# Kernel tuning notes

Hardware: AMD Instinct MI355X
Metric: run time of the kernel (lower is better)

## Reference

```python
import jax, jax.numpy as jnp
import numpy as np

J_NUM = 24
# SMPL kinematic tree: parents[i] < i for all i >= 1 (root has parent -1)
PARENTS = np.array([-1, 0, 0, 0, 1, 2, 3, 4, 5, 6, 7, 8, 9, 9, 9, 12, 13, 14,
                    16, 17, 18, 19, 20, 21], dtype=np.int32)
BATCH = 131072


def setup_inputs() -> dict:
    key = jax.random.key(0)
    k1, k2, k3 = jax.random.split(key, 3)
    pose = jax.random.normal(k1, (BATCH, J_NUM, 3), dtype=jnp.float32) * 0.3
    trans = jax.random.normal(k2, (BATCH, 3), dtype=jnp.float32)
    # Rest-pose joint transforms: identity rotation + random local offset (learned buffer)
    offs = jax.random.normal(k3, (J_NUM, 3), dtype=jnp.float32) * 0.1
    J = jnp.tile(jnp.eye(4, dtype=jnp.float32)[None], (J_NUM, 1, 1))
    J = J.at[:, :3, 3].set(offs)
    parents = jnp.asarray(PARENTS, dtype=jnp.int32)
    return {"pose": pose, "trans": trans, "J": J, "parents": parents}


def rodrigues(r):
    """Axis-angle [..., 3] -> rotation matrices [..., 3, 3] (batched Rodrigues)."""
    theta = jnp.sqrt(jnp.sum(r * r, axis=-1, keepdims=True) + 1e-16)  # [...,1]
    rh = r / theta
    x, y, z = rh[..., 0], rh[..., 1], rh[..., 2]
    zero = jnp.zeros_like(x)
    K = jnp.stack([zero, -z, y, z, zero, -x, -y, x, zero], axis=-1)
    K = K.reshape(r.shape[:-1] + (3, 3))
    c = jnp.cos(theta)[..., None]
    s = jnp.sin(theta)[..., None]
    outer = rh[..., :, None] * rh[..., None, :]
    I3 = jnp.eye(3, dtype=r.dtype)
    return c * I3 + (1.0 - c) * outer + s * K


def reference(pose, trans, J, parents):
    par = np.asarray(parents)  # static tree structure
    B, Jn = pose.shape[0], pose.shape[1]
    R = rodrigues(pose)                                   # [B,J,3,3]
    # embed into 4x4 homogeneous transforms
    R4 = jnp.pad(R, ((0, 0), (0, 0), (0, 1), (0, 1)))
    R4 = R4.at[:, :, 3, 3].set(1.0)                       # [B,J,4,4]
    # local transform per joint: J[i] @ localRot[i] (batched once)
    local = jnp.einsum('jab,njbc->njac', J, R4)           # [B,J,4,4]
    # sequential kinematic-tree composition (fixed small unrolled loop)
    results = [local[:, 0]]
    for i in range(1, Jn):
        results.append(jnp.matmul(results[int(par[i])], local[:, i]))
    stacked = jnp.stack(results, axis=1)                  # [B,J,4,4]
    J_posed = stacked[:, :, :3, 3] + trans[:, None, :]    # [B,J,3]
    return J_posed
```

## Files before the change

kernel.cpp:

```cpp
#include <hip/hip_runtime.h>

#define J_NUM 24
#define ELEMS 64
#define NTHREADS (ELEMS * 3)
#define STRIDE 73

__global__ __launch_bounds__(NTHREADS)
void fk_kernel(const float* __restrict__ pose, const float* __restrict__ trans,
               const float* __restrict__ Jm, float* __restrict__ out)
{
    __shared__ float s[ELEMS * STRIDE];

    const int u = threadIdx.x;
    const size_t blockBase = (size_t)blockIdx.x * ELEMS;

    {
        const float4* src = reinterpret_cast<const float4*>(pose + blockBase * 72);
#pragma unroll
        for (int i = 0; i < 6; ++i) {
            int m = i * NTHREADS + u;
            float4 v = src[m];
            int e = m / 18;
            int f = (m - e * 18) * 4;
            float* d = s + e * STRIDE + f;
            d[0] = v.x; d[1] = v.y; d[2] = v.z; d[3] = v.w;
        }
    }

    const float tr = trans[blockBase * 3 + u];

    __syncthreads();

    const int e = u / 3;
    const int r = u - e * 3;
    const float* p = s + e * STRIDE;

    const int par[J_NUM] = {-1,0,0,0,1,2,3,4,5,6,7,8,9,9,9,12,13,14,16,17,18,19,20,21};

    float rcx[J_NUM], rcy[J_NUM], rcz[J_NUM];
    float pc[J_NUM];

#pragma unroll
    for (int j = 0; j < J_NUM; ++j) {
        float ax = p[j*3+0], ay = p[j*3+1], az = p[j*3+2];
        float tt = ax*ax + ay*ay + az*az + 1e-16f;
        float inv = rsqrtf(tt);
        float th = tt * inv;
        float x = ax*inv, y = ay*inv, z = az*inv;
        float c = __cosf(th), sn = __sinf(th);
        float C = 1.0f - c;
        float cx = C*x, cy = C*y, cz = C*z;
        float sx = sn*x, sy = sn*y, sz = sn*z;
        float R0 = fmaf(cx, x, c);
        float R1 = fmaf(cx, y, -sz);
        float R2 = fmaf(cx, z,  sy);
        float R3 = fmaf(cy, x,  sz);
        float R4 = fmaf(cy, y, c);
        float R5 = fmaf(cy, z, -sx);
        float R6 = fmaf(cz, x, -sy);
        float R7 = fmaf(cz, y,  sx);
        float R8 = fmaf(cz, z, c);

        float ox = Jm[j*16 + 3];
        float oy = Jm[j*16 + 7];
        float oz = Jm[j*16 + 11];

        if (j == 0) {
            rcx[0] = (r == 0) ? R0 : ((r == 1) ? R3 : R6);
            rcy[0] = (r == 0) ? R1 : ((r == 1) ? R4 : R7);
            rcz[0] = (r == 0) ? R2 : ((r == 1) ? R5 : R8);
            pc[0]  = (r == 0) ? ox : ((r == 1) ? oy : oz);
        } else {
            const int q = par[j];
            float c0 = rcx[q], c1 = rcy[q], c2 = rcz[q];
            pc[j]  = pc[q] + c0*ox + c1*oy + c2*oz;
            rcx[j] = c0*R0 + c1*R3 + c2*R6;
            rcy[j] = c0*R1 + c1*R4 + c2*R7;
            rcz[j] = c0*R2 + c1*R5 + c2*R8;
        }
    }

    __syncthreads();

    {
        float* w = s + e * STRIDE + r;
#pragma unroll
        for (int j = 0; j < J_NUM; ++j)
            w[j*3] = pc[j] + tr;
    }

    __syncthreads();

    {
        float4* dst = reinterpret_cast<float4*>(out + blockBase * 72);
#pragma unroll
        for (int i = 0; i < 6; ++i) {
            int m = i * NTHREADS + u;
            int e2 = m / 18;
            int f = (m - e2 * 18) * 4;
            const float* src = s + e2 * STRIDE + f;
            float4 v;
            v.x = src[0]; v.y = src[1]; v.z = src[2]; v.w = src[3];
            dst[m] = v;
        }
    }
}

extern "C" void kernel_launch(void* const* d_in, const int* in_sizes, int n_in,
                              void* d_out, int out_size, void* d_ws, size_t ws_size,
                              hipStream_t stream) {
    const float* pose  = (const float*)d_in[0];
    const float* trans = (const float*)d_in[1];
    const float* Jm    = (const float*)d_in[2];
    float* out = (float*)d_out;

    int B = in_sizes[0] / (J_NUM * 3);
    int blocks = B / ELEMS;
    fk_kernel<<<blocks, NTHREADS, 0, stream>>>(pose, trans, Jm, out);
}
```

Measured before the change: 96.13 us.

## Map one batch element per thread and load pose directly to registers

```diff
diff --git a/kernel.cpp b/kernel.cpp
--- a/kernel.cpp
+++ b/kernel.cpp
@@ -1,51 +1,45 @@
 #include <hip/hip_runtime.h>
 
 #define J_NUM 24
-#define ELEMS 64
-#define NTHREADS (ELEMS * 3)
-#define STRIDE 73
+#define BLOCK 64
+#define STRIDE 76
 
-__global__ __launch_bounds__(NTHREADS)
+__global__ __launch_bounds__(BLOCK, 2)
 void fk_kernel(const float* __restrict__ pose, const float* __restrict__ trans,
                const float* __restrict__ Jm, float* __restrict__ out)
 {
-    __shared__ float s[ELEMS * STRIDE];
+    __shared__ __align__(16) float s[BLOCK * STRIDE];
 
-    const int u = threadIdx.x;
-    const size_t blockBase = (size_t)blockIdx.x * ELEMS;
+    const int t = threadIdx.x;
+    const size_t blockBase = (size_t)blockIdx.x * BLOCK;
+    const size_t b = blockBase + t;
 
+    float p[72];
     {
-        const float4* src = reinterpret_cast<const float4*>(pose + blockBase * 72);
+        const float4* pp = reinterpret_cast<const float4*>(pose + b * 72);
 #pragma unroll
-        for (int i = 0; i < 6; ++i) {
-            int m = i * NTHREADS + u;
-            float4 v = src[m];
-            int e = m / 18;
-            int f = (m - e * 18) * 4;
-            float* d = s + e * STRIDE + f;
-            d[0] = v.x; d[1] = v.y; d[2] = v.z; d[3] = v.w;
+        for (int i = 0; i < 18; ++i) {
+            float4 v = pp[i];
+            p[4*i+0] = v.x; p[4*i+1] = v.y; p[4*i+2] = v.z; p[4*i+3] = v.w;
         }
     }
 
-    const float tr = trans[blockBase * 3 + u];
-
-    __syncthreads();
-
-    const int e = u / 3;
-    const int r = u - e * 3;
-    const float* p = s + e * STRIDE;
+    const float t0 = trans[b*3 + 0];
+    const float t1 = trans[b*3 + 1];
+    const float t2 = trans[b*3 + 2];
 
     const int par[J_NUM] = {-1,0,0,0,1,2,3,4,5,6,7,8,9,9,9,12,13,14,16,17,18,19,20,21};
 
-    float rcx[J_NUM], rcy[J_NUM], rcz[J_NUM];
-    float pc[J_NUM];
+    float Rc[J_NUM][9];
+    float Pc[J_NUM][3];
+    float o[72];
 
 #pragma unroll
     for (int j = 0; j < J_NUM; ++j) {
         float ax = p[j*3+0], ay = p[j*3+1], az = p[j*3+2];
-        float tt = ax*ax + ay*ay + az*az + 1e-16f;
+        float tt = fmaf(ax, ax, fmaf(ay, ay, fmaf(az, az, 1e-16f)));
         float inv = rsqrtf(tt);
-        float th = tt * inv;
+        float th  = tt * inv;
         float x = ax*inv, y = ay*inv, z = az*inv;
         float c = __cosf(th), sn = __sinf(th);
         float C = 1.0f - c;
@@ -66,27 +60,39 @@
         float oz = Jm[j*16 + 11];
 
         if (j == 0) {
-            rcx[0] = (r == 0) ? R0 : ((r == 1) ? R3 : R6);
-            rcy[0] = (r == 0) ? R1 : ((r == 1) ? R4 : R7);
-            rcz[0] = (r == 0) ? R2 : ((r == 1) ? R5 : R8);
-            pc[0]  = (r == 0) ? ox : ((r == 1) ? oy : oz);
+            Rc[0][0]=R0; Rc[0][1]=R1; Rc[0][2]=R2;
+            Rc[0][3]=R3; Rc[0][4]=R4; Rc[0][5]=R5;
+            Rc[0][6]=R6; Rc[0][7]=R7; Rc[0][8]=R8;
+            Pc[0][0]=ox; Pc[0][1]=oy; Pc[0][2]=oz;
         } else {
             const int q = par[j];
-            float c0 = rcx[q], c1 = rcy[q], c2 = rcz[q];
-            pc[j]  = pc[q] + c0*ox + c1*oy + c2*oz;
-            rcx[j] = c0*R0 + c1*R3 + c2*R6;
-            rcy[j] = c0*R1 + c1*R4 + c2*R7;
-            rcz[j] = c0*R2 + c1*R5 + c2*R8;
+            Pc[j][0] = fmaf(Rc[q][0], ox, fmaf(Rc[q][1], oy, fmaf(Rc[q][2], oz, Pc[q][0])));
+            Pc[j][1] = fmaf(Rc[q][3], ox, fmaf(Rc[q][4], oy, fmaf(Rc[q][5], oz, Pc[q][1])));
+            Pc[j][2] = fmaf(Rc[q][6], ox, fmaf(Rc[q][7], oy, fmaf(Rc[q][8], oz, Pc[q][2])));
+            Rc[j][0] = fmaf(Rc[q][0], R0, fmaf(Rc[q][1], R3, Rc[q][2]*R6));
+            Rc[j][1] = fmaf(Rc[q][0], R1, fmaf(Rc[q][1], R4, Rc[q][2]*R7));
+            Rc[j][2] = fmaf(Rc[q][0], R2, fmaf(Rc[q][1], R5, Rc[q][2]*R8));
+            Rc[j][3] = fmaf(Rc[q][3], R0, fmaf(Rc[q][4], R3, Rc[q][5]*R6));
+            Rc[j][4] = fmaf(Rc[q][3], R1, fmaf(Rc[q][4], R4, Rc[q][5]*R7));
+            Rc[j][5] = fmaf(Rc[q][3], R2, fmaf(Rc[q][4], R5, Rc[q][5]*R8));
+            Rc[j][6] = fmaf(Rc[q][6], R0, fmaf(Rc[q][7], R3, Rc[q][8]*R6));
+            Rc[j][7] = fmaf(Rc[q][6], R1, fmaf(Rc[q][7], R4, Rc[q][8]*R7));
+            Rc[j][8] = fmaf(Rc[q][6], R2, fmaf(Rc[q][7], R5, Rc[q][8]*R8));
         }
+
+        o[j*3+0] = Pc[j][0] + t0;
+        o[j*3+1] = Pc[j][1] + t1;
+        o[j*3+2] = Pc[j][2] + t2;
     }
 
-    __syncthreads();
-
     {
-        float* w = s + e * STRIDE + r;
+        float* mine = s + t * STRIDE;
 #pragma unroll
-        for (int j = 0; j < J_NUM; ++j)
-            w[j*3] = pc[j] + tr;
+        for (int k = 0; k < 18; ++k) {
+            float4 v;
+            v.x = o[4*k+0]; v.y = o[4*k+1]; v.z = o[4*k+2]; v.w = o[4*k+3];
+            *reinterpret_cast<float4*>(mine + 4*k) = v;
+        }
     }
 
     __syncthreads();
@@ -94,13 +100,11 @@
     {
         float4* dst = reinterpret_cast<float4*>(out + blockBase * 72);
 #pragma unroll
-        for (int i = 0; i < 6; ++i) {
-            int m = i * NTHREADS + u;
-            int e2 = m / 18;
-            int f = (m - e2 * 18) * 4;
-            const float* src = s + e2 * STRIDE + f;
-            float4 v;
-            v.x = src[0]; v.y = src[1]; v.z = src[2]; v.w = src[3];
+        for (int i = 0; i < 18; ++i) {
+            int m = i * BLOCK + t;
+            int e = m / 18;
+            int f = (m - e * 18) * 4;
+            float4 v = *reinterpret_cast<const float4*>(s + e * STRIDE + f);
             dst[m] = v;
         }
     }
@@ -115,6 +119,6 @@
     float* out = (float*)d_out;
 
     int B = in_sizes[0] / (J_NUM * 3);
-    int blocks = B / ELEMS;
-    fk_kernel<<<blocks, NTHREADS, 0, stream>>>(pose, trans, Jm, out);
+    int blocks = B / BLOCK;
+    fk_kernel<<<blocks, BLOCK, 0, stream>>>(pose, trans, Jm, out);
 }
```

After: 94.33 us. About the same (-1.9%).
